# Kernel tuning notes

Hardware: AMD Instinct MI355X
Metric: run time of the kernel (lower is better)

The kernel has to match this reference:

```python
import jax, jax.numpy as jnp
import numpy as np

B, T, WIN, CIN, H, COUT = 512, 64, 256, 4, 512, 2


def setup_inputs() -> dict:
    key = jax.random.key(0)
    k = jax.random.split(key, 4)
    D = WIN * CIN  # 1024
    s = 0.02
    return {
        "inputs": jax.random.normal(k[0], (B, T, WIN, CIN), dtype=jnp.float32),
        "W_in": jax.random.normal(k[1], (D, 3 * H), dtype=jnp.float32) * s,
        "b_in": jnp.zeros((3 * H,), dtype=jnp.float32),
        "U": jax.random.normal(k[2], (H, 3 * H), dtype=jnp.float32) * s,
        "b_rec": jnp.zeros((3 * H,), dtype=jnp.float32),
        "W2": jax.random.normal(k[3], (2 * H, WIN * COUT), dtype=jnp.float32) * s,
        "b2": jnp.zeros((WIN * COUT,), dtype=jnp.float32),
    }


def _gru_last_state(x, W_in, b_in, U, b_rec):
    # Keras GRU v2 math: reset_after=True, recurrent_activation=sigmoid,
    # activation=relu (as configured). training=False -> no dropout.
    Bm, Tm, _ = x.shape
    Hm = U.shape[0]
    # precompute input projections for all timesteps: [B, T, 3H]
    xg = jnp.einsum("btd,dh->bth", x, W_in) + b_in

    def step(h, xg_t):
        hg = h @ U + b_rec  # recurrent bias applied before reset gate (reset_after)
        xz, xr, xh = jnp.split(xg_t, 3, axis=-1)
        hz, hr, hh = jnp.split(hg, 3, axis=-1)
        z = jax.nn.sigmoid(xz + hz)
        r = jax.nn.sigmoid(xr + hr)
        h_cand = jax.nn.relu(xh + r * hh)
        h_new = z * h + (1.0 - z) * h_cand
        return h_new, None

    h0 = jnp.zeros((Bm, Hm), dtype=x.dtype)
    hT, _ = jax.lax.scan(step, h0, jnp.swapaxes(xg, 0, 1))
    return hT  # [B, H]; with return_sequences=False, output == final_state


def reference(inputs, W_in, b_in, U, b_rec, W2, b2):
    Bm, Tm = inputs.shape[0], inputs.shape[1]
    x = inputs.reshape(Bm, Tm, -1)  # flatten window*channels -> [B, T, 1024]
    hT = _gru_last_state(x, W_in, b_in, U, b_rec)
    cat = jnp.concatenate([hT, hT], axis=-1)  # tf.concat((output, final_state))
    out = cat @ W2 + b2
    return out.reshape(Bm, WIN, COUT)
```

## Files before the change

### kernel.cpp

```cpp
#include <hip/hip_runtime.h>
#include <hip/hip_bf16.h>
#include <stdint.h>

#define BATCH 512
#define TSTEPS 64
#define DIN 1024
#define HID 512
#define G3 1536
#define MROWS (BATCH * TSTEPS)
#define POUT 512

typedef __attribute__((ext_vector_type(8))) short bf16x8;
typedef __attribute__((ext_vector_type(4))) float f32x4;

__device__ __forceinline__ float bf2f(short s) {
  union { unsigned u; float f; } v;
  v.u = ((unsigned)(unsigned short)s) << 16;
  return v.f;
}
__device__ __forceinline__ short f2bf(float f) {
  __hip_bfloat16 h = __float2bfloat16(f);
  short s;
  __builtin_memcpy(&s, &h, 2);
  return s;
}
__device__ __forceinline__ void gload_lds16(const void* g, void* l) {
  __builtin_amdgcn_global_load_lds(
      (const __attribute__((address_space(1))) void*)g,
      (__attribute__((address_space(3))) void*)l, 16, 0, 0);
}

__global__ __launch_bounds__(256) void transpose_cast(const float* __restrict__ in,
                                                      short* __restrict__ out,
                                                      int R, int C) {
  __shared__ float tile[32][33];
  const int c0 = blockIdx.x * 32, r0 = blockIdx.y * 32;
  const int tx = threadIdx.x & 31, ty = threadIdx.x >> 5;
#pragma unroll
  for (int i = 0; i < 4; ++i) {
    const int r = r0 + ty + i * 8;
    tile[ty + i * 8][tx] = in[(size_t)r * C + c0 + tx];
  }
  __syncthreads();
#pragma unroll
  for (int i = 0; i < 4; ++i) {
    const int c = c0 + ty + i * 8;
    out[(size_t)c * R + r0 + tx] = f2bf(tile[tx][ty + i * 8]);
  }
}

__global__ __launch_bounds__(256) void u_pack2(const float* __restrict__ U,
                                               short* __restrict__ Upk) {
  const unsigned idx = blockIdx.x * 256 + threadIdx.x;
  const unsigned cg = idx / 49152u;
  const unsigned rem = idx - cg * 49152u;
  const unsigned ur = rem >> 9;
  const unsigned r2 = rem & 511u;
  const unsigned s = r2 >> 3, e = r2 & 7u;
  const unsigned chunk = s ^ (ur & 7u);
  const unsigned k = chunk * 8u + e;
  const unsigned g = ur >> 5, cc = ur & 31u;
  const unsigned col = g * 512u + cg * 32u + cc;
  Upk[idx] = f2bf(U[(size_t)k * G3 + col]);
}

__global__ __launch_bounds__(256) void gemm_xg_mfma(const float* __restrict__ X,
                                                    const short* __restrict__ Wt,
                                                    const float* __restrict__ bin,
                                                    __hip_bfloat16* __restrict__ XG) {
  __shared__ __align__(16) short As[128 * 64];
  __shared__ __align__(16) short Bs[128 * 64];
  const int tid = threadIdx.x;
  const int w = tid >> 6, l = tid & 63;
  const int lc = l & 15, lg = l >> 4;

  const int xcd = blockIdx.x & 7;
  const int idx = blockIdx.x >> 3;
  const int wg = xcd * 384 + idx;
  const int rt = wg / 12, ct = wg % 12;
  const int row0 = rt * 128, col0 = ct * 128;

  const int wm = w >> 1, wn = w & 1;

  f32x4 acc[4][4];
#pragma unroll
  for (int mt = 0; mt < 4; ++mt)
#pragma unroll
    for (int nt = 0; nt < 4; ++nt) acc[mt][nt] = (f32x4){0.f, 0.f, 0.f, 0.f};

  const int tr = tid >> 3, p = tid & 7;

  for (int k0 = 0; k0 < DIN; k0 += 64) {
    float4 ar[4][2];
#pragma unroll
    for (int i = 0; i < 4; ++i) {
      const int r = i * 32 + tr;
      const int s = p ^ (r & 7);
      const float* xp = &X[(size_t)(row0 + r) * DIN + k0 + s * 8];
      ar[i][0] = *reinterpret_cast<const float4*>(xp);
      ar[i][1] = *reinterpret_cast<const float4*>(xp + 4);
    }
    __syncthreads();
#pragma unroll
    for (int i = 0; i < 4; ++i) {
      const int r = i * 32 + tr;
      bf16x8 v;
      v[0] = f2bf(ar[i][0].x); v[1] = f2bf(ar[i][0].y);
      v[2] = f2bf(ar[i][0].z); v[3] = f2bf(ar[i][0].w);
      v[4] = f2bf(ar[i][1].x); v[5] = f2bf(ar[i][1].y);
      v[6] = f2bf(ar[i][1].z); v[7] = f2bf(ar[i][1].w);
      *reinterpret_cast<bf16x8*>((char*)As + r * 128 + p * 16) = v;
    }
#pragma unroll
    for (int i = 0; i < 4; ++i) {
      const int rr = w * 32 + i * 8 + (l >> 3);
      const int pp = l & 7;
      const int s = pp ^ (rr & 7);
      gload_lds16(&Wt[(size_t)(col0 + rr) * DIN + k0 + s * 8],
                  (char*)Bs + (w * 32 + i * 8) * 128);
    }
    __syncthreads();
#pragma unroll
    for (int kc = 0; kc < 2; ++kc) {
      bf16x8 a[4], b[4];
#pragma unroll
      for (int mt = 0; mt < 4; ++mt) {
        const int R = wm * 64 + mt * 16 + lc;
        const int ch = (kc * 4 + lg) ^ (R & 7);
        a[mt] = *reinterpret_cast<const bf16x8*>((const char*)As + R * 128 + ch * 16);
      }
#pragma unroll
      for (int nt = 0; nt < 4; ++nt) {
        const int Rn = wn * 64 + nt * 16 + lc;
        const int ch = (kc * 4 + lg) ^ (Rn & 7);
        b[nt] = *reinterpret_cast<const bf16x8*>((const char*)Bs + Rn * 128 + ch * 16);
      }
#pragma unroll
      for (int mt = 0; mt < 4; ++mt)
#pragma unroll
        for (int nt = 0; nt < 4; ++nt)
          acc[mt][nt] = __builtin_amdgcn_mfma_f32_16x16x32_bf16(a[mt], b[nt],
                                                                acc[mt][nt], 0, 0, 0);
    }
  }

  float bv[4];
#pragma unroll
  for (int nt = 0; nt < 4; ++nt) bv[nt] = bin[col0 + wn * 64 + nt * 16 + lc];
#pragma unroll
  for (int mt = 0; mt < 4; ++mt) {
#pragma unroll
    for (int nt = 0; nt < 4; ++nt) {
      const int col = col0 + wn * 64 + nt * 16 + lc;
      const int g = col >> 9, cgc = (col >> 5) & 15, cc = col & 31;
#pragma unroll
      for (int rr = 0; rr < 4; ++rr) {
        const int m = row0 + wm * 64 + mt * 16 + lg * 4 + rr;
        const int t = m & 63, b = m >> 6;
        const size_t o =
            ((((size_t)t * 16 + (b >> 5)) * 16 + cgc) * 32 + (b & 31)) * 96 +
            g * 32 + cc;
        XG[o] = __float2bfloat16(acc[mt][nt][rr] + bv[nt]);
      }
    }
  }
}

__global__ __launch_bounds__(256) void gru_scan_coop(
    const __hip_bfloat16* __restrict__ XG, const short* __restrict__ Upk,
    const float* __restrict__ brec, short* h_g, unsigned* bar,
    float* __restrict__ HT) {
  __shared__ __align__(16) short Us[96 * 512];
  __shared__ __align__(16) short hS[32 * 512];
  __shared__ __align__(16) short xgL[2][3072];
  const int tid = threadIdx.x, w = tid >> 6, l = tid & 63;
  const int lc = l & 15, lg = l >> 4;
  const int bg = blockIdx.x >> 4, cgi = blockIdx.x & 15;
  const int b0 = bg * 32, c0 = cgi * 32;
  const int wm = w >> 1, wn = w & 1;
  unsigned* const flags = bar + bg * 16;

  {
    const short* usrc = Upk + (size_t)cgi * 49152;
#pragma unroll
    for (int r = 0; r < 24; ++r)
      gload_lds16(usrc + (r * 256 + tid) * 8, Us + (r * 256 + (tid & ~63)) * 8);
  }
  for (int i = tid; i < 4096; i += 256) ((unsigned long long*)hS)[i] = 0ull;

  const short* XGs = (const short*)XG;
  {
    const short* xs = XGs + (size_t)bg * 49152 + (size_t)cgi * 3072;
    gload_lds16(xs + tid * 8, (char*)xgL[0] + w * 1024);
    if (tid < 128)
      gload_lds16(xs + (256 + tid) * 8, (char*)xgL[0] + 4096 + w * 1024);
  }

  const int j = c0 + wn * 16 + lc;
  const float brz = brec[j], brr = brec[512 + j], brh = brec[1024 + j];
  const int arow = wm * 16 + lc;
  const int ur0 = wn * 16 + lc;

  __syncthreads();

  for (int t = 0; t < TSTEPS; ++t) {
    f32x4 za0 = (f32x4){0.f, 0.f, 0.f, 0.f}, za1 = za0, za2 = za0;
    if (t > 0) {
      for (;;) {
        const unsigned f = __hip_atomic_load(&flags[l & 15], __ATOMIC_RELAXED,
                                             __HIP_MEMORY_SCOPE_AGENT);
        if (__all((int)(f >= (unsigned)t))) break;
        __builtin_amdgcn_s_sleep(1);
      }
      const unsigned long long* hsrc = (const unsigned long long*)(
          h_g + ((size_t)(t & 1) * BATCH + b0) * 512);
      unsigned long long v[16];
#pragma unroll
      for (int r = 0; r < 16; ++r)
        v[r] = __hip_atomic_load(hsrc + r * 256 + tid, __ATOMIC_RELAXED,
                                 __HIP_MEMORY_SCOPE_AGENT);
#pragma unroll
      for (int r = 0; r < 16; ++r)
        ((unsigned long long*)hS)[r * 256 + tid] = v[r];
      __syncthreads();

#pragma unroll
      for (int kc = 0; kc < 16; ++kc) {
        const int s = kc * 4 + lg;
        const bf16x8 a = *(const bf16x8*)((const char*)hS + arow * 1024 +
                                          ((s ^ (arow & 7)) << 4));
        const char* ub = (const char*)Us + ur0 * 1024 + ((s ^ (ur0 & 7)) << 4);
        const bf16x8 bz = *(const bf16x8*)(ub);
        const bf16x8 brg = *(const bf16x8*)(ub + 32 * 1024);
        const bf16x8 bh = *(const bf16x8*)(ub + 64 * 1024);
        za0 = __builtin_amdgcn_mfma_f32_16x16x32_bf16(a, bz, za0, 0, 0, 0);
        za1 = __builtin_amdgcn_mfma_f32_16x16x32_bf16(a, brg, za1, 0, 0, 0);
        za2 = __builtin_amdgcn_mfma_f32_16x16x32_bf16(a, bh, za2, 0, 0, 0);
      }
    }

    const short* xb = xgL[t & 1];
#pragma unroll
    for (int r = 0; r < 4; ++r) {
      const int lb = wm * 16 + lg * 4 + r;
      const float xz = bf2f(xb[lb * 96 + wn * 16 + lc]);
      const float xr = bf2f(xb[lb * 96 + 32 + wn * 16 + lc]);
      const float xh = bf2f(xb[lb * 96 + 64 + wn * 16 + lc]);
      const float z = 1.f / (1.f + __expf(-(xz + za0[r] + brz)));
      const float rg = 1.f / (1.f + __expf(-(xr + za1[r] + brr)));
      const float hc = fmaxf(fmaf(rg, za2[r] + brh, xh), 0.f);
      const int hoff = lb * 1024 + (((j >> 3) ^ (lb & 7)) << 4) + (j & 7) * 2;
      const float hold = bf2f(*(const short*)((const char*)hS + hoff));
      const float hnew = fmaf(z, hold - hc, hc);
      if (t == TSTEPS - 1) {
        HT[(size_t)(b0 + lb) * HID + j] = hnew;
      } else {
        __hip_atomic_store(
            (unsigned short*)((char*)h_g +
                              ((size_t)((t + 1) & 1) * BATCH + b0) * 1024 + hoff),
            (unsigned short)f2bf(hnew), __ATOMIC_RELAXED,
            __HIP_MEMORY_SCOPE_AGENT);
      }
    }
    if (t == TSTEPS - 1) break;

    __syncthreads();
    if (tid == 0)
      __hip_atomic_store(&flags[cgi], (unsigned)(t + 1), __ATOMIC_RELAXED,
                         __HIP_MEMORY_SCOPE_AGENT);
    {
      const short* xs = XGs + ((size_t)(t + 1) * 16 + (size_t)bg) * 49152 +
                        (size_t)cgi * 3072;
      char* xd = (char*)xgL[(t + 1) & 1];
      gload_lds16(xs + tid * 8, xd + w * 1024);
      if (tid < 128)
        gload_lds16(xs + (256 + tid) * 8, xd + 4096 + w * 1024);
    }
  }
}

__global__ __launch_bounds__(256) void final_proj(const float* __restrict__ HT,
                                                  const float* __restrict__ W2,
                                                  const float* __restrict__ b2,
                                                  float* __restrict__ OUT) {
  const int b = blockIdx.x >> 1;
  const int pp = ((blockIdx.x & 1) << 8) + threadIdx.x;
  float acc = b2[pp];
  const float* h = &HT[(size_t)b * HID];
  for (int k = 0; k < HID; ++k)
    acc = fmaf(h[k], W2[(size_t)k * POUT + pp] + W2[(size_t)(k + HID) * POUT + pp], acc);
  OUT[(size_t)b * POUT + pp] = acc;
}

extern "C" void kernel_launch(void* const* d_in, const int* in_sizes, int n_in,
                              void* d_out, int out_size, void* d_ws,
                              size_t ws_size, hipStream_t stream) {
  const float* X    = (const float*)d_in[0];
  const float* Win  = (const float*)d_in[1];
  const float* bin  = (const float*)d_in[2];
  const float* U    = (const float*)d_in[3];
  const float* brec = (const float*)d_in[4];
  const float* W2   = (const float*)d_in[5];
  const float* b2   = (const float*)d_in[6];
  float* OUT = (float*)d_out;

  char* ws = (char*)d_ws;
  size_t off = 0;
  __hip_bfloat16* XG = (__hip_bfloat16*)(ws + off); off += (size_t)MROWS * G3 * 2;
  short* Wt   = (short*)(ws + off); off += (size_t)G3 * DIN * 2;
  short* Upk  = (short*)(ws + off); off += (size_t)G3 * HID * 2;
  float* HT   = (float*)(ws + off); off += (size_t)BATCH * HID * 4;
  short* h_g  = (short*)(ws + off); off += (size_t)2 * BATCH * HID * 2;
  unsigned* bar = (unsigned*)(ws + off);

  hipMemsetAsync(bar, 0, 1024, stream);

  transpose_cast<<<dim3(G3 / 32, DIN / 32), 256, 0, stream>>>(Win, Wt, DIN, G3);
  u_pack2<<<(16 * 96 * 512) / 256, 256, 0, stream>>>(U, Upk);
  gemm_xg_mfma<<<(MROWS / 128) * (G3 / 128), 256, 0, stream>>>(X, Wt, bin, XG);

  const __hip_bfloat16* XGc = XG;
  const short* Upkc = Upk;
  void* args[] = {(void*)&XGc, (void*)&Upkc, (void*)&brec,
                  (void*)&h_g, (void*)&bar, (void*)&HT};
  hipLaunchCooperativeKernel((const void*)gru_scan_coop, dim3(256), dim3(256),
                             args, 0, stream);

  final_proj<<<(BATCH * POUT) / 256, 256, 0, stream>>>(HT, W2, b2, OUT);
}
```

Before: 485.5 us.

## Use counter barrier and coalesced 8-byte hidden-state exchange in GRU scan

Replaces the per-block flag array polled by a whole wavefront with a single atomic counter per batch group that only thread 0 polls and fetch-adds. New hidden values are staged in LDS and then written to global as coalesced 8-byte stores instead of scattered 2-byte atomic stores. The global h layout becomes unswizzled, and the swizzle is applied when loading into LDS. This adds an extra __syncthreads per step and serialises the 16 blocks on one contended counter.

```diff
diff --git a/kernel.cpp b/kernel.cpp
--- a/kernel.cpp
+++ b/kernel.cpp
@@ -178,7 +178,7 @@
   const int bg = blockIdx.x >> 4, cgi = blockIdx.x & 15;
   const int b0 = bg * 32, c0 = cgi * 32;
   const int wm = w >> 1, wn = w & 1;
-  unsigned* const flags = bar + bg * 16;
+  unsigned* const cnt = bar + bg * 16;
 
   {
     const short* usrc = Upk + (size_t)cgi * 49152;
@@ -200,18 +200,23 @@
   const float brz = brec[j], brr = brec[512 + j], brh = brec[1024 + j];
   const int arow = wm * 16 + lc;
   const int ur0 = wn * 16 + lc;
+  const int lb2 = tid >> 3, qq = tid & 7;
+  const int cpo_ch = ((c0 >> 3) + (qq >> 1)) ^ (lb2 & 7);
+  const int cpo_lds = lb2 * 1024 + (cpo_ch << 4) + (qq & 1) * 8;
+  const size_t cpo_g = (size_t)(b0 + lb2) * 1024 + (size_t)(c0 + qq * 4) * 2;
 
   __syncthreads();
 
   for (int t = 0; t < TSTEPS; ++t) {
     f32x4 za0 = (f32x4){0.f, 0.f, 0.f, 0.f}, za1 = za0, za2 = za0;
     if (t > 0) {
-      for (;;) {
-        const unsigned f = __hip_atomic_load(&flags[l & 15], __ATOMIC_RELAXED,
-                                             __HIP_MEMORY_SCOPE_AGENT);
-        if (__all((int)(f >= (unsigned)t))) break;
-        __builtin_amdgcn_s_sleep(1);
-      }
+      if (tid == 0) {
+        const unsigned tgt = 16u * (unsigned)t;
+        while (__hip_atomic_load(cnt, __ATOMIC_RELAXED,
+                                 __HIP_MEMORY_SCOPE_AGENT) < tgt)
+          __builtin_amdgcn_s_sleep(1);
+      }
+      __syncthreads();
       const unsigned long long* hsrc = (const unsigned long long*)(
           h_g + ((size_t)(t & 1) * BATCH + b0) * 512);
       unsigned long long v[16];
@@ -220,8 +225,14 @@
         v[r] = __hip_atomic_load(hsrc + r * 256 + tid, __ATOMIC_RELAXED,
                                  __HIP_MEMORY_SCOPE_AGENT);
 #pragma unroll
-      for (int r = 0; r < 16; ++r)
-        ((unsigned long long*)hS)[r * 256 + tid] = v[r];
+      for (int r = 0; r < 16; ++r) {
+        const int idxq = r * 256 + tid;
+        const int row = idxq >> 7;
+        const int i7 = idxq & 127;
+        const int ch = (i7 >> 1) ^ (row & 7);
+        *(unsigned long long*)((char*)hS + row * 1024 + (ch << 4) +
+                               (i7 & 1) * 8) = v[r];
+      }
       __syncthreads();
 
 #pragma unroll
@@ -255,19 +266,24 @@
       if (t == TSTEPS - 1) {
         HT[(size_t)(b0 + lb) * HID + j] = hnew;
       } else {
-        __hip_atomic_store(
-            (unsigned short*)((char*)h_g +
-                              ((size_t)((t + 1) & 1) * BATCH + b0) * 1024 + hoff),
-            (unsigned short)f2bf(hnew), __ATOMIC_RELAXED,
-            __HIP_MEMORY_SCOPE_AGENT);
+        *(short*)((char*)hS + hoff) = f2bf(hnew);
       }
     }
     if (t == TSTEPS - 1) break;
 
+    __syncthreads();
+    {
+      const unsigned long long hv =
+          *(const unsigned long long*)((const char*)hS + cpo_lds);
+      __hip_atomic_store(
+          (unsigned long long*)((char*)h_g +
+                                (size_t)((t + 1) & 1) * BATCH * 1024 + cpo_g),
+          hv, __ATOMIC_RELAXED, __HIP_MEMORY_SCOPE_AGENT);
+    }
     __syncthreads();
     if (tid == 0)
-      __hip_atomic_store(&flags[cgi], (unsigned)(t + 1), __ATOMIC_RELAXED,
-                         __HIP_MEMORY_SCOPE_AGENT);
+      __hip_atomic_fetch_add(cnt, 1u, __ATOMIC_RELAXED,
+                             __HIP_MEMORY_SCOPE_AGENT);
     {
       const short* xs = XGs + ((size_t)(t + 1) * 16 + (size_t)bg) * 49152 +
                         (size_t)cgi * 3072;
@@ -316,7 +332,7 @@
   hipMemsetAsync(bar, 0, 1024, stream);
 
   transpose_cast<<<dim3(G3 / 32, DIN / 32), 256, 0, stream>>>(Win, Wt, DIN, G3);
-  u_pack2<<<(16 * 96 * 512) / 256, 256, 0, stream>>>(U, Upk);
+  u_pack2<<<(HID * G3) / 256, 256, 0, stream>>>(U, Upk);
   gemm_xg_mfma<<<(MROWS / 128) * (G3 / 128), 256, 0, stream>>>(X, Wt, bin, XG);
 
   const __hip_bfloat16* XGc = XG;
```

Result: no change. 490.7 us (+1.1%).

## Keep recurrent weights in registers and halve scan grid to 128 blocks of 512

Applied to the files above, without the earlier changes.

The GRU scan now keeps each wave's slice of U permanently in VGPRs (48 bf16x8 vectors per lane) instead of staging it in LDS, removing per-step LDS reads of U. The grid changes from 256 blocks of 256 threads to 128 blocks of 512 threads, with each block covering 64 hidden columns, so fewer blocks take part in each barrier group (8 per batch group instead of 16). U packing and the XG output layout are reworked to match the new column grouping. This brings heavy register pressure, which may spill or limit occupancy, and each block now does more work per step.

```diff
diff --git a/kernel.cpp b/kernel.cpp
--- a/kernel.cpp
+++ b/kernel.cpp
@@ -50,18 +50,19 @@
 }
 
 __global__ __launch_bounds__(256) void u_pack2(const float* __restrict__ U,
-                                               short* __restrict__ Upk) {
+                                               short* __restrict__ Upk2) {
   const unsigned idx = blockIdx.x * 256 + threadIdx.x;
-  const unsigned cg = idx / 49152u;
-  const unsigned rem = idx - cg * 49152u;
-  const unsigned ur = rem >> 9;
-  const unsigned r2 = rem & 511u;
-  const unsigned s = r2 >> 3, e = r2 & 7u;
-  const unsigned chunk = s ^ (ur & 7u);
-  const unsigned k = chunk * 8u + e;
-  const unsigned g = ur >> 5, cc = ur & 31u;
-  const unsigned col = g * 512u + cg * 32u + cc;
-  Upk[idx] = f2bf(U[(size_t)k * G3 + col]);
+  const unsigned e = idx & 7u;
+  unsigned tmp = idx >> 3;
+  const unsigned lc = tmp & 15u; tmp >>= 4;
+  const unsigned lg = tmp & 3u;  tmp >>= 2;
+  const unsigned wn = tmp & 3u;  tmp >>= 2;
+  const unsigned f = tmp % 48u;
+  const unsigned cg = tmp / 48u;
+  const unsigned g = f >> 4, kc = f & 15u;
+  const unsigned k = kc * 32u + lg * 8u + e;
+  const unsigned col = g * 512u + cg * 64u + wn * 16u + lc;
+  Upk2[idx] = f2bf(U[(size_t)k * G3 + col]);
 }
 
 __global__ __launch_bounds__(256) void gemm_xg_mfma(const float* __restrict__ X,
@@ -152,54 +153,57 @@
 #pragma unroll
     for (int nt = 0; nt < 4; ++nt) {
       const int col = col0 + wn * 64 + nt * 16 + lc;
-      const int g = col >> 9, cgc = (col >> 5) & 15, cc = col & 31;
+      const int g = col >> 9;
+      const int rem = col & 511;
+      const int cgc = rem >> 6, cc = rem & 63;
 #pragma unroll
       for (int rr = 0; rr < 4; ++rr) {
         const int m = row0 + wm * 64 + mt * 16 + lg * 4 + rr;
         const int t = m & 63, b = m >> 6;
         const size_t o =
-            ((((size_t)t * 16 + (b >> 5)) * 16 + cgc) * 32 + (b & 31)) * 96 +
-            g * 32 + cc;
+            ((((size_t)t * 16 + (b >> 5)) * 8 + cgc) * 32 + (b & 31)) * 192 +
+            g * 64 + cc;
         XG[o] = __float2bfloat16(acc[mt][nt][rr] + bv[nt]);
       }
     }
   }
 }
 
-__global__ __launch_bounds__(256) void gru_scan_coop(
-    const __hip_bfloat16* __restrict__ XG, const short* __restrict__ Upk,
+__global__ __launch_bounds__(512, 2) void gru_scan_coop(
+    const __hip_bfloat16* __restrict__ XG, const short* __restrict__ Upk2,
     const float* __restrict__ brec, short* h_g, unsigned* bar,
     float* __restrict__ HT) {
-  __shared__ __align__(16) short Us[96 * 512];
   __shared__ __align__(16) short hS[32 * 512];
-  __shared__ __align__(16) short xgL[2][3072];
+  __shared__ __align__(16) short xgL[2][6144];
   const int tid = threadIdx.x, w = tid >> 6, l = tid & 63;
   const int lc = l & 15, lg = l >> 4;
-  const int bg = blockIdx.x >> 4, cgi = blockIdx.x & 15;
-  const int b0 = bg * 32, c0 = cgi * 32;
-  const int wm = w >> 1, wn = w & 1;
+  const int bg = blockIdx.x >> 3, cgi = blockIdx.x & 7;
+  const int b0 = bg * 32, c0 = cgi * 64;
+  const int wm = w & 1, wn = w >> 1;
   unsigned* const flags = bar + bg * 16;
 
-  {
-    const short* usrc = Upk + (size_t)cgi * 49152;
-#pragma unroll
-    for (int r = 0; r < 24; ++r)
-      gload_lds16(usrc + (r * 256 + tid) * 8, Us + (r * 256 + (tid & ~63)) * 8);
-  }
-  for (int i = tid; i < 4096; i += 256) ((unsigned long long*)hS)[i] = 0ull;
+  bf16x8 ub[3][16];
+#pragma unroll
+  for (int g = 0; g < 3; ++g)
+#pragma unroll
+    for (int kc = 0; kc < 16; ++kc)
+      ub[g][kc] = *reinterpret_cast<const bf16x8*>(
+          Upk2 + ((((size_t)cgi * 48 + g * 16 + kc) * 4 + wn) * 4 + lg) * 128 +
+          lc * 8);
+
+  for (int i = tid; i < 4096; i += 512) ((unsigned long long*)hS)[i] = 0ull;
 
   const short* XGs = (const short*)XG;
   {
-    const short* xs = XGs + (size_t)bg * 49152 + (size_t)cgi * 3072;
+    const short* xs = XGs + ((size_t)bg * 8 + cgi) * 6144;
     gload_lds16(xs + tid * 8, (char*)xgL[0] + w * 1024);
-    if (tid < 128)
-      gload_lds16(xs + (256 + tid) * 8, (char*)xgL[0] + 4096 + w * 1024);
+    if (tid < 256)
+      gload_lds16(xs + (512 + tid) * 8, (char*)xgL[0] + 8192 + w * 1024);
   }
 
   const int j = c0 + wn * 16 + lc;
   const float brz = brec[j], brr = brec[512 + j], brh = brec[1024 + j];
   const int arow = wm * 16 + lc;
-  const int ur0 = wn * 16 + lc;
 
   __syncthreads();
 
@@ -207,21 +211,21 @@
     f32x4 za0 = (f32x4){0.f, 0.f, 0.f, 0.f}, za1 = za0, za2 = za0;
     if (t > 0) {
       for (;;) {
-        const unsigned f = __hip_atomic_load(&flags[l & 15], __ATOMIC_RELAXED,
+        const unsigned f = __hip_atomic_load(&flags[l & 7], __ATOMIC_RELAXED,
                                              __HIP_MEMORY_SCOPE_AGENT);
         if (__all((int)(f >= (unsigned)t))) break;
         __builtin_amdgcn_s_sleep(1);
       }
       const unsigned long long* hsrc = (const unsigned long long*)(
           h_g + ((size_t)(t & 1) * BATCH + b0) * 512);
-      unsigned long long v[16];
-#pragma unroll
-      for (int r = 0; r < 16; ++r)
-        v[r] = __hip_atomic_load(hsrc + r * 256 + tid, __ATOMIC_RELAXED,
+      unsigned long long v[8];
+#pragma unroll
+      for (int r = 0; r < 8; ++r)
+        v[r] = __hip_atomic_load(hsrc + r * 512 + tid, __ATOMIC_RELAXED,
                                  __HIP_MEMORY_SCOPE_AGENT);
 #pragma unroll
-      for (int r = 0; r < 16; ++r)
-        ((unsigned long long*)hS)[r * 256 + tid] = v[r];
+      for (int r = 0; r < 8; ++r)
+        ((unsigned long long*)hS)[r * 512 + tid] = v[r];
       __syncthreads();
 
 #pragma unroll
@@ -229,13 +233,9 @@
         const int s = kc * 4 + lg;
         const bf16x8 a = *(const bf16x8*)((const char*)hS + arow * 1024 +
                                           ((s ^ (arow & 7)) << 4));
-        const char* ub = (const char*)Us + ur0 * 1024 + ((s ^ (ur0 & 7)) << 4);
-        const bf16x8 bz = *(const bf16x8*)(ub);
-        const bf16x8 brg = *(const bf16x8*)(ub + 32 * 1024);
-        const bf16x8 bh = *(const bf16x8*)(ub + 64 * 1024);
-        za0 = __builtin_amdgcn_mfma_f32_16x16x32_bf16(a, bz, za0, 0, 0, 0);
-        za1 = __builtin_amdgcn_mfma_f32_16x16x32_bf16(a, brg, za1, 0, 0, 0);
-        za2 = __builtin_amdgcn_mfma_f32_16x16x32_bf16(a, bh, za2, 0, 0, 0);
+        za0 = __builtin_amdgcn_mfma_f32_16x16x32_bf16(a, ub[0][kc], za0, 0, 0, 0);
+        za1 = __builtin_amdgcn_mfma_f32_16x16x32_bf16(a, ub[1][kc], za1, 0, 0, 0);
+        za2 = __builtin_amdgcn_mfma_f32_16x16x32_bf16(a, ub[2][kc], za2, 0, 0, 0);
       }
     }
 
@@ -243,9 +243,9 @@
 #pragma unroll
     for (int r = 0; r < 4; ++r) {
       const int lb = wm * 16 + lg * 4 + r;
-      const float xz = bf2f(xb[lb * 96 + wn * 16 + lc]);
-      const float xr = bf2f(xb[lb * 96 + 32 + wn * 16 + lc]);
-      const float xh = bf2f(xb[lb * 96 + 64 + wn * 16 + lc]);
+      const float xz = bf2f(xb[lb * 192 + wn * 16 + lc]);
+      const float xr = bf2f(xb[lb * 192 + 64 + wn * 16 + lc]);
+      const float xh = bf2f(xb[lb * 192 + 128 + wn * 16 + lc]);
       const float z = 1.f / (1.f + __expf(-(xz + za0[r] + brz)));
       const float rg = 1.f / (1.f + __expf(-(xr + za1[r] + brr)));
       const float hc = fmaxf(fmaf(rg, za2[r] + brh, xh), 0.f);
@@ -269,12 +269,11 @@
       __hip_atomic_store(&flags[cgi], (unsigned)(t + 1), __ATOMIC_RELAXED,
                          __HIP_MEMORY_SCOPE_AGENT);
     {
-      const short* xs = XGs + ((size_t)(t + 1) * 16 + (size_t)bg) * 49152 +
-                        (size_t)cgi * 3072;
+      const short* xs = XGs + (((size_t)(t + 1) * 16 + bg) * 8 + cgi) * 6144;
       char* xd = (char*)xgL[(t + 1) & 1];
       gload_lds16(xs + tid * 8, xd + w * 1024);
-      if (tid < 128)
-        gload_lds16(xs + (256 + tid) * 8, xd + 4096 + w * 1024);
+      if (tid < 256)
+        gload_lds16(xs + (512 + tid) * 8, xd + 8192 + w * 1024);
     }
   }
 }
@@ -308,7 +307,7 @@
   size_t off = 0;
   __hip_bfloat16* XG = (__hip_bfloat16*)(ws + off); off += (size_t)MROWS * G3 * 2;
   short* Wt   = (short*)(ws + off); off += (size_t)G3 * DIN * 2;
-  short* Upk  = (short*)(ws + off); off += (size_t)G3 * HID * 2;
+  short* Upk2 = (short*)(ws + off); off += (size_t)G3 * HID * 2;
   float* HT   = (float*)(ws + off); off += (size_t)BATCH * HID * 4;
   short* h_g  = (short*)(ws + off); off += (size_t)2 * BATCH * HID * 2;
   unsigned* bar = (unsigned*)(ws + off);
@@ -316,14 +315,14 @@
   hipMemsetAsync(bar, 0, 1024, stream);
 
   transpose_cast<<<dim3(G3 / 32, DIN / 32), 256, 0, stream>>>(Win, Wt, DIN, G3);
-  u_pack2<<<(16 * 96 * 512) / 256, 256, 0, stream>>>(U, Upk);
+  u_pack2<<<(HID * G3) / 256, 256, 0, stream>>>(U, Upk2);
   gemm_xg_mfma<<<(MROWS / 128) * (G3 / 128), 256, 0, stream>>>(X, Wt, bin, XG);
 
   const __hip_bfloat16* XGc = XG;
-  const short* Upkc = Upk;
+  const short* Upkc = Upk2;
   void* args[] = {(void*)&XGc, (void*)&Upkc, (void*)&brec,
                   (void*)&h_g, (void*)&bar, (void*)&HT};
-  hipLaunchCooperativeKernel((const void*)gru_scan_coop, dim3(256), dim3(256),
+  hipLaunchCooperativeKernel((const void*)gru_scan_coop, dim3(128), dim3(512),
                              args, 0, stream);
 
   final_proj<<<(BATCH * POUT) / 256, 256, 0, stream>>>(HT, W2, b2, OUT);
```

Result: faster. 470.6 us (-3.1%).
